# Performance work log

Hardware: AMD Instinct MI355X
Metric: run time of the kernel (lower is better)

The kernel has to match this reference:

```python
import jax, jax.numpy as jnp
import numpy as np

SAMPLE_RATE = 48000
MIX = 0.5
DELAYS_SEC = [0.0297, 0.0371, 0.0411, 0.0437, 0.0533, 0.0617, 0.0731, 0.0797]
DELAYS = [int(d * SAMPLE_RATE) for d in DELAYS_SEC]  # integer sample delays
N = len(DELAYS)
T = 8388608  # ~175 s of mono audio at 48 kHz


def setup_inputs() -> dict:
    key = jax.random.key(0)
    k1, k2, k3 = jax.random.split(key, 3)
    input_sig = jax.random.normal(k1, (1, T), dtype=jnp.float32)
    feedback_gain = jax.random.uniform(k2, (N,), dtype=jnp.float32)
    # orthogonal mix matrix via QR of a random Gaussian, as in the module's __init__
    rm = np.asarray(jax.random.normal(k3, (N, N), dtype=jnp.float32))
    q, _ = np.linalg.qr(rm)
    orthogonal_matrix = jnp.asarray(q, dtype=jnp.float32)
    return {"input_sig": input_sig, "feedback_gain": feedback_gain,
            "orthogonal_matrix": orthogonal_matrix}


def reference(input_sig, feedback_gain, orthogonal_matrix):
    x = input_sig[0]  # [T]
    # Delay buffers start at zero, so each delay line's output is the input
    # shifted right by `d` samples and zero-padded at the front.
    shifted = jnp.stack(
        [jnp.concatenate([jnp.zeros((d,), x.dtype), x[: x.shape[0] - d]]) for d in DELAYS],
        axis=0)  # [N, T]
    # sum_j (Q @ (g[:,None]*shifted))[j] == (ones @ Q) * g  dotted with shifted rows
    combined = (jnp.sum(orthogonal_matrix, axis=0) * feedback_gain)  # [N]
    wet = jnp.einsum('n,nt->t', combined, shifted)[None, :]  # [1, T]
    out = wet * MIX + input_sig * (1.0 - MIX)
    out = out / jnp.max(jnp.abs(out))
    return out
```

## Files before the change

### kernel.cpp

```cpp
#include <hip/hip_runtime.h>

#define T_LEN 8388608
#define NTAPS 8
#define CHUNK 4096
#define HALO  3840
#define LDSF  (HALO + CHUNK)

#define D0 1425
#define D1 1780
#define D2 1972
#define D3 2097
#define D4 2558
#define D5 2961
#define D6 3508
#define D7 3825

__global__ __launch_bounds__(256) void fdn_pass1(
    const float* __restrict__ x, const float* __restrict__ g,
    const float* __restrict__ Q, float* __restrict__ out,
    unsigned int* __restrict__ maxbits) {
    __shared__ __align__(16) float smem[LDSF];
    __shared__ float csh[NTAPS];
    __shared__ float wmax[4];

    const int tid = threadIdx.x;

    if (tid < NTAPS) {
        float s = 0.f;
#pragma unroll
        for (int j = 0; j < NTAPS; ++j) s += Q[j * NTAPS + tid];
        csh[tid] = s * g[tid];
    }

    const long gs = (long)blockIdx.x * CHUNK - HALO;
    for (int v = tid; v < LDSF / 4; v += 256) {
        long ga = gs + (long)v * 4;
        float4 val;
        if (ga >= 0) val = *(const float4*)(x + ga);
        else         val = make_float4(0.f, 0.f, 0.f, 0.f);
        *(float4*)(smem + v * 4) = val;
    }
    __syncthreads();

    float c0 = csh[0], c1 = csh[1], c2 = csh[2], c3 = csh[3];
    float c4 = csh[4], c5 = csh[5], c6 = csh[6], c7 = csh[7];

    const int base = blockIdx.x * CHUNK;
    float m = 0.f;
#pragma unroll
    for (int i = 0; i < CHUNK / 256; ++i) {
        const int j = i * 256 + tid;
        const float* p = smem + HALO + j;
        float wet = 0.f;
        wet = fmaf(c0, p[-D0], wet);
        wet = fmaf(c1, p[-D1], wet);
        wet = fmaf(c2, p[-D2], wet);
        wet = fmaf(c3, p[-D3], wet);
        wet = fmaf(c4, p[-D4], wet);
        wet = fmaf(c5, p[-D5], wet);
        wet = fmaf(c6, p[-D6], wet);
        wet = fmaf(c7, p[-D7], wet);
        float v = fmaf(0.5f, wet, 0.5f * p[0]);
        out[base + j] = v;
        m = fmaxf(m, fabsf(v));
    }

#pragma unroll
    for (int off = 32; off > 0; off >>= 1) m = fmaxf(m, __shfl_down(m, off, 64));
    if ((tid & 63) == 0) wmax[tid >> 6] = m;
    __syncthreads();
    if (tid == 0) {
        float bm = fmaxf(fmaxf(wmax[0], wmax[1]), fmaxf(wmax[2], wmax[3]));
        atomicMax(maxbits, __float_as_uint(bm));
    }
}

__global__ __launch_bounds__(256) void fdn_scale(
    float* __restrict__ out, const unsigned int* __restrict__ maxbits) {
    const float inv = 1.0f / __uint_as_float(*maxbits);
    const int i = (blockIdx.x * 256 + threadIdx.x) * 4;
    float4 v = *(const float4*)(out + i);
    v.x *= inv; v.y *= inv; v.z *= inv; v.w *= inv;
    *(float4*)(out + i) = v;
}

extern "C" void kernel_launch(void* const* d_in, const int* in_sizes, int n_in,
                              void* d_out, int out_size, void* d_ws, size_t ws_size,
                              hipStream_t stream) {
    const float* x = (const float*)d_in[0];
    const float* g = (const float*)d_in[1];
    const float* Q = (const float*)d_in[2];
    float* out = (float*)d_out;
    unsigned int* maxbits = (unsigned int*)d_ws;

    hipMemsetAsync(d_ws, 0, sizeof(unsigned int), stream);

    fdn_pass1<<<dim3(T_LEN / CHUNK), dim3(256), 0, stream>>>(x, g, Q, out, maxbits);
    fdn_scale<<<dim3(T_LEN / (256 * 4)), dim3(256), 0, stream>>>(out, maxbits);
}
```

Baseline: 119.6 us.

## Fuse max normalization into a single cooperative kernel with a grid sync

Replaces the two-kernel pipeline (tap sum with atomic max, then a separate rescale pass) and the memset with one cooperative kernel of 512 large blocks. Each block keeps its 64 outputs per thread in registers, publishes a per-block max, syncs the grid, reduces all block maxima, and writes the scaled output once. This removes the extra read and write pass over the output and two launch overheads. In exchange it brings a grid-wide barrier, much larger LDS tiles that allow only two blocks per CU and so less latency hiding, and a stride-4 LDS access pattern that may cause bank conflicts.

```diff
diff --git a/kernel.cpp b/kernel.cpp
--- a/kernel.cpp
+++ b/kernel.cpp
@@ -1,8 +1,12 @@
 #include <hip/hip_runtime.h>
+#include <hip/hip_cooperative_groups.h>
+
+namespace cg = cooperative_groups;
 
 #define T_LEN 8388608
 #define NTAPS 8
-#define CHUNK 4096
+#define NBLK  512
+#define CHUNK (T_LEN / NBLK)
 #define HALO  3840
 #define LDSF  (HALO + CHUNK)
 
@@ -15,15 +19,17 @@
 #define D6 3508
 #define D7 3825
 
-__global__ __launch_bounds__(256) void fdn_pass1(
+__global__ __launch_bounds__(256, 2) void fdn_fused(
     const float* __restrict__ x, const float* __restrict__ g,
     const float* __restrict__ Q, float* __restrict__ out,
-    unsigned int* __restrict__ maxbits) {
+    float* __restrict__ wsf) {
     __shared__ __align__(16) float smem[LDSF];
     __shared__ float csh[NTAPS];
     __shared__ float wmax[4];
+    __shared__ float sinv;
 
     const int tid = threadIdx.x;
+    const int blk = blockIdx.x;
 
     if (tid < NTAPS) {
         float s = 0.f;
@@ -32,37 +38,39 @@
         csh[tid] = s * g[tid];
     }
 
-    const long gs = (long)blockIdx.x * CHUNK - HALO;
-    for (int v = tid; v < LDSF / 4; v += 256) {
-        long ga = gs + (long)v * 4;
-        float4 val;
+    const long gs = (long)blk * CHUNK - HALO;
+    for (int v4 = tid; v4 < LDSF / 4; v4 += 256) {
+        long ga = gs + (long)v4 * 4;
+        float4 val = make_float4(0.f, 0.f, 0.f, 0.f);
         if (ga >= 0) val = *(const float4*)(x + ga);
-        else         val = make_float4(0.f, 0.f, 0.f, 0.f);
-        *(float4*)(smem + v * 4) = val;
+        *(float4*)(smem + v4 * 4) = val;
     }
     __syncthreads();
 
-    float c0 = csh[0], c1 = csh[1], c2 = csh[2], c3 = csh[3];
-    float c4 = csh[4], c5 = csh[5], c6 = csh[6], c7 = csh[7];
+    const float c0 = csh[0], c1 = csh[1], c2 = csh[2], c3 = csh[3];
+    const float c4 = csh[4], c5 = csh[5], c6 = csh[6], c7 = csh[7];
 
-    const int base = blockIdx.x * CHUNK;
+    float v[CHUNK / 256];
     float m = 0.f;
 #pragma unroll
-    for (int i = 0; i < CHUNK / 256; ++i) {
-        const int j = i * 256 + tid;
+    for (int i = 0; i < CHUNK / 1024; ++i) {
+        const int j = i * 1024 + tid * 4;
         const float* p = smem + HALO + j;
-        float wet = 0.f;
-        wet = fmaf(c0, p[-D0], wet);
-        wet = fmaf(c1, p[-D1], wet);
-        wet = fmaf(c2, p[-D2], wet);
-        wet = fmaf(c3, p[-D3], wet);
-        wet = fmaf(c4, p[-D4], wet);
-        wet = fmaf(c5, p[-D5], wet);
-        wet = fmaf(c6, p[-D6], wet);
-        wet = fmaf(c7, p[-D7], wet);
-        float v = fmaf(0.5f, wet, 0.5f * p[0]);
-        out[base + j] = v;
-        m = fmaxf(m, fabsf(v));
+#pragma unroll
+        for (int k = 0; k < 4; ++k) {
+            float wet = 0.f;
+            wet = fmaf(c0, p[k - D0], wet);
+            wet = fmaf(c1, p[k - D1], wet);
+            wet = fmaf(c2, p[k - D2], wet);
+            wet = fmaf(c3, p[k - D3], wet);
+            wet = fmaf(c4, p[k - D4], wet);
+            wet = fmaf(c5, p[k - D5], wet);
+            wet = fmaf(c6, p[k - D6], wet);
+            wet = fmaf(c7, p[k - D7], wet);
+            float o = fmaf(0.5f, wet, 0.5f * p[k]);
+            v[i * 4 + k] = o;
+            m = fmaxf(m, fabsf(o));
+        }
     }
 
 #pragma unroll
@@ -71,17 +79,31 @@
     __syncthreads();
     if (tid == 0) {
         float bm = fmaxf(fmaxf(wmax[0], wmax[1]), fmaxf(wmax[2], wmax[3]));
-        atomicMax(maxbits, __float_as_uint(bm));
+        __hip_atomic_store(wsf + blk, bm, __ATOMIC_RELEASE, __HIP_MEMORY_SCOPE_AGENT);
     }
-}
 
-__global__ __launch_bounds__(256) void fdn_scale(
-    float* __restrict__ out, const unsigned int* __restrict__ maxbits) {
-    const float inv = 1.0f / __uint_as_float(*maxbits);
-    const int i = (blockIdx.x * 256 + threadIdx.x) * 4;
-    float4 v = *(const float4*)(out + i);
-    v.x *= inv; v.y *= inv; v.z *= inv; v.w *= inv;
-    *(float4*)(out + i) = v;
+    cg::this_grid().sync();
+
+    float a = __hip_atomic_load(wsf + tid,       __ATOMIC_ACQUIRE, __HIP_MEMORY_SCOPE_AGENT);
+    float b = __hip_atomic_load(wsf + tid + 256, __ATOMIC_ACQUIRE, __HIP_MEMORY_SCOPE_AGENT);
+    float mm = fmaxf(a, b);
+#pragma unroll
+    for (int off = 32; off > 0; off >>= 1) mm = fmaxf(mm, __shfl_down(mm, off, 64));
+    if ((tid & 63) == 0) wmax[tid >> 6] = mm;
+    __syncthreads();
+    if (tid == 0)
+        sinv = 1.0f / fmaxf(fmaxf(wmax[0], wmax[1]), fmaxf(wmax[2], wmax[3]));
+    __syncthreads();
+    const float inv = sinv;
+
+    const int base = blk * CHUNK;
+#pragma unroll
+    for (int i = 0; i < CHUNK / 1024; ++i) {
+        const int j = i * 1024 + tid * 4;
+        float4 ov = make_float4(v[i * 4 + 0] * inv, v[i * 4 + 1] * inv,
+                                v[i * 4 + 2] * inv, v[i * 4 + 3] * inv);
+        *(float4*)(out + base + j) = ov;
+    }
 }
 
 extern "C" void kernel_launch(void* const* d_in, const int* in_sizes, int n_in,
@@ -91,10 +113,9 @@
     const float* g = (const float*)d_in[1];
     const float* Q = (const float*)d_in[2];
     float* out = (float*)d_out;
-    unsigned int* maxbits = (unsigned int*)d_ws;
+    float* wsf = (float*)d_ws;
 
-    hipMemsetAsync(d_ws, 0, sizeof(unsigned int), stream);
-
-    fdn_pass1<<<dim3(T_LEN / CHUNK), dim3(256), 0, stream>>>(x, g, Q, out, maxbits);
-    fdn_scale<<<dim3(T_LEN / (256 * 4)), dim3(256), 0, stream>>>(out, maxbits);
+    void* args[] = {(void*)&x, (void*)&g, (void*)&Q, (void*)&out, (void*)&wsf};
+    hipLaunchCooperativeKernel((const void*)fdn_fused, dim3(NBLK), dim3(256),
+                               args, 0, stream);
 }
```

After: 204.0 us. 70.6% more time.
